# Kernel tuning notes

Hardware: AMD Instinct MI355X
Metric: run time of the kernel (lower is better)

Reference implementation:

```python
import jax, jax.numpy as jnp
import numpy as np

N_HEAD = 16
R = 4  # reciprocal rank

def setup_inputs() -> dict:
    key = jax.random.key(0)
    ks = jax.random.split(key, 8)
    B, T, C = 2, 2048, 1024
    H = N_HEAD
    D = C // H
    D_std = D - R
    x = jax.random.normal(ks[0], (B, T, C), dtype=jnp.float32)
    W_attn = jax.random.normal(ks[1], (3 * C, C), dtype=jnp.float32) * (1.0 / np.sqrt(C))
    W_proj = jax.random.normal(ks[2], (C, C), dtype=jnp.float32) * (1.0 / np.sqrt(C))
    w_std = jnp.full((H,), D_std / D, dtype=jnp.float32)
    w_rec = jnp.full((H,), R / D, dtype=jnp.float32)
    skip_std = jnp.float32(2.0)
    skip_low = jnp.float32(-3.0)
    rwr_alpha = jnp.full((H,), 0.05, dtype=jnp.float32)
    return {"x": x, "W_attn": W_attn, "W_proj": W_proj, "w_std": w_std,
            "w_rec": w_rec, "skip_std": skip_std, "skip_low": skip_low,
            "rwr_alpha": rwr_alpha}

def reference(x, W_attn, W_proj, w_std, w_rec, skip_std, skip_low, rwr_alpha):
    B, T, C = x.shape
    H = N_HEAD
    D = C // H
    D_std = D - R
    # fused QKV projection: [Qf | Kf | V]
    fused = jnp.einsum('btc,fc->btf', x, W_attn)
    qf, kf, v = jnp.split(fused, 3, axis=-1)
    Qf = qf.reshape(B, T, H, D).transpose(0, 2, 1, 3)  # (B,H,T,D)
    Kf = kf.reshape(B, T, H, D).transpose(0, 2, 1, 3)
    V = v.reshape(B, T, H, D).transpose(0, 2, 1, 3)
    # dynamic per-head gate scaling folded into Qf/Kf
    g_std = jnp.sqrt(jnp.clip(w_std * jax.nn.sigmoid(skip_std), 1e-8))  # (H,)
    g_rec = jnp.sqrt(jnp.clip(w_rec * jax.nn.sigmoid(skip_low), 1e-8))  # (H,)
    scale = jnp.concatenate([
        jnp.broadcast_to(g_std[:, None], (H, D_std)),
        jnp.broadcast_to(g_rec[:, None], (H, R)),
    ], axis=-1)  # (H, D)
    scale = scale[None, :, None, :]  # (1,H,1,D)
    Qf = Qf * scale
    Kf = Kf * scale
    # causal SDPA (scale = 1/sqrt(head_dim), dropout=0)
    scores = jnp.einsum('bhqd,bhkd->bhqk', Qf, Kf) / jnp.sqrt(jnp.float32(D))
    causal = jnp.tril(jnp.ones((T, T), dtype=bool))
    scores = jnp.where(causal[None, None], scores, jnp.float32(-1e30))
    attn = jax.nn.softmax(scores, axis=-1)
    y = jnp.einsum('bhqk,bhkd->bhqd', attn, V)
    # self-restart mix: out = (1-alpha)*attn_out + alpha*V, alpha in [0, 0.5]
    alpha = jnp.clip(rwr_alpha, 0.0, 0.5)[None, :, None, None]
    y = (1.0 - alpha) * y + alpha * V
    y = y.transpose(0, 2, 1, 3).reshape(B, T, C)
    return jnp.einsum('btc,oc->bto', y, W_proj)
```

## Files before the change

### kernel.cpp

```cpp
#include <hip/hip_runtime.h>
#include <hip/hip_bf16.h>
#include <math.h>
#include <stdint.h>

#define B_    2
#define T_    2048
#define C_    1024
#define H_    16
#define D_    64
#define R_    4
#define DSTD  60
#define F_    3072
#define BT_   (B_ * T_)

#define LOG2E 1.44269504088896340736f

typedef __bf16 bf16x8 __attribute__((ext_vector_type(8)));
typedef __bf16 bf16x4 __attribute__((ext_vector_type(4)));
typedef float  f32x4  __attribute__((ext_vector_type(4)));

__device__ __forceinline__ int swz(int row, int blk) {
    return blk ^ ((row >> 1) & 7);
}

__device__ __forceinline__ void st_pair(__bf16* p, __bf16 a, __bf16 b) {
    union { __bf16 h[2]; uint32_t u; } t;
    t.h[0] = a; t.h[1] = b;
    *(uint32_t*)p = t.u;
}

__device__ __forceinline__ void gload_lds16(const void* g, void* l) {
    __builtin_amdgcn_global_load_lds(
        (const __attribute__((address_space(1))) uint32_t*)g,
        (__attribute__((address_space(3))) uint32_t*)l, 16, 0, 0);
}

__global__ __launch_bounds__(256) void cast3_kernel(
    const float* __restrict__ a, int na4,
    const float* __restrict__ b, int nb4,
    const float* __restrict__ c, int nc4,
    __bf16* __restrict__ oa, __bf16* __restrict__ ob, __bf16* __restrict__ oc)
{
    int i = blockIdx.x * 256 + threadIdx.x;
    const float* s; __bf16* d; int j = i;
    if (j < na4) { s = a; d = oa; }
    else {
        j -= na4;
        if (j < nb4) { s = b; d = ob; }
        else {
            j -= nb4;
            if (j >= nc4) return;
            s = c; d = oc;
        }
    }
    float4 v = ((const float4*)s)[j];
    bf16x4 o;
    o[0] = (__bf16)v.x; o[1] = (__bf16)v.y;
    o[2] = (__bf16)v.z; o[3] = (__bf16)v.w;
    ((bf16x4*)d)[j] = o;
}

__global__ __launch_bounds__(256) void gemm_qkv_kernel(
    const __bf16* __restrict__ A,
    const __bf16* __restrict__ Bw,
    const float* __restrict__ w_std, const float* __restrict__ w_rec,
    const float* __restrict__ skip_std, const float* __restrict__ skip_low,
    __bf16* __restrict__ Q, __bf16* __restrict__ K, __bf16* __restrict__ V)
{
    __shared__ __bf16 As[128 * 64];
    __shared__ __bf16 Bs[128 * 64];

    const int tid  = threadIdx.x;
    const int row0 = blockIdx.x * 128;
    const int col0 = blockIdx.y * 128;

    const int w    = tid >> 6;
    const int lane = tid & 63;
    const int quad = lane >> 4;
    const int lt   = lane & 15;
    const int wm   = w >> 1;
    const int wn   = w & 1;

    const int srow = tid >> 3;
    const int sblk = tid & 7;

    f32x4 acc[4][4];
#pragma unroll
    for (int i = 0; i < 4; ++i)
#pragma unroll
        for (int j = 0; j < 4; ++j)
#pragma unroll
            for (int r = 0; r < 4; ++r) acc[i][j][r] = 0.f;

    for (int kt = 0; kt < C_ / 64; ++kt) {
        const int k0 = kt * 64;
        __syncthreads();
#pragma unroll
        for (int cc = 0; cc < 4; ++cc) {
            const int r  = cc * 32 + srow;
            const int sb = sblk ^ ((r >> 1) & 7);
            gload_lds16(A  + (size_t)(row0 + r) * C_ + k0 + sb * 8,
                        As + cc * 2048 + tid * 8);
            gload_lds16(Bw + (size_t)(col0 + r) * C_ + k0 + sb * 8,
                        Bs + cc * 2048 + tid * 8);
        }
        __syncthreads();

        bf16x8 waf[2][4], xf[2][4];
#pragma unroll
        for (int kk = 0; kk < 2; ++kk)
#pragma unroll
            for (int i = 0; i < 4; ++i) {
                const int rf = wn * 64 + i * 16 + lt;
                waf[kk][i] = *(const bf16x8*)&Bs[rf * 64 + swz(rf, kk * 4 + quad) * 8];
                const int rt = wm * 64 + i * 16 + lt;
                xf[kk][i]  = *(const bf16x8*)&As[rt * 64 + swz(rt, kk * 4 + quad) * 8];
            }
#pragma unroll
        for (int kk = 0; kk < 2; ++kk)
#pragma unroll
            for (int i = 0; i < 4; ++i)
#pragma unroll
                for (int j = 0; j < 4; ++j)
                    acc[i][j] = __builtin_amdgcn_mfma_f32_16x16x32_bf16(
                        waf[kk][i], xf[kk][j], acc[i][j], 0, 0, 0);
    }

    const int colbase = col0 + wn * 64;
    const int which   = colbase >> 10;
    const int h       = (colbase & (C_ - 1)) >> 6;

    const float ss = 1.f / (1.f + __expf(-skip_std[0]));
    const float sl = 1.f / (1.f + __expf(-skip_low[0]));
    const float gs = sqrtf(fmaxf(w_std[h] * ss, 1e-8f));
    const float gr = sqrtf(fmaxf(w_rec[h] * sl, 1e-8f));

    __bf16* dstM = (which == 0) ? Q : (which == 1) ? K : V;

#pragma unroll
    for (int i = 0; i < 4; ++i) {
        const int d0 = i * 16 + quad * 4;
        float sc = (d0 < DSTD) ? gs : gr;
        if (which == 0) sc *= 0.125f * LOG2E;
        const bool scale = (which != 2);
#pragma unroll
        for (int j = 0; j < 4; ++j) {
            const int trow = row0 + wm * 64 + j * 16 + lt;
            const int b = trow >> 11;
            const int t = trow & (T_ - 1);
            bf16x4 o;
#pragma unroll
            for (int r = 0; r < 4; ++r) {
                float v = acc[i][j][r];
                if (scale) v *= sc;
                o[r] = (__bf16)v;
            }
            *(bf16x4*)(dstM + (((size_t)b * H_ + h) * T_ + t) * D_ + d0) = o;
        }
    }
}

__global__ __launch_bounds__(256) void gemm_out_kernel(
    const __bf16* __restrict__ A,
    const __bf16* __restrict__ Bw,
    float* __restrict__ out)
{
    __shared__ __bf16 As[128 * 64];
    __shared__ __bf16 Bs[64 * 64];

    const int tid  = threadIdx.x;
    const int row0 = blockIdx.x * 128;
    const int col0 = blockIdx.y * 64;

    const int w    = tid >> 6;
    const int lane = tid & 63;
    const int quad = lane >> 4;
    const int lt   = lane & 15;
    const int wm   = w >> 1;
    const int wn   = w & 1;

    const int srow = tid >> 3;
    const int sblk = tid & 7;

    f32x4 acc[2][4];
#pragma unroll
    for (int i = 0; i < 2; ++i)
#pragma unroll
        for (int j = 0; j < 4; ++j)
#pragma unroll
            for (int r = 0; r < 4; ++r) acc[i][j][r] = 0.f;

    for (int kt = 0; kt < C_ / 64; ++kt) {
        const int k0 = kt * 64;
        __syncthreads();
#pragma unroll
        for (int cc = 0; cc < 4; ++cc) {
            const int r  = cc * 32 + srow;
            const int sb = sblk ^ ((r >> 1) & 7);
            gload_lds16(A + (size_t)(row0 + r) * C_ + k0 + sb * 8,
                        As + cc * 2048 + tid * 8);
        }
#pragma unroll
        for (int cc = 0; cc < 2; ++cc) {
            const int r  = cc * 32 + srow;
            const int sb = sblk ^ ((r >> 1) & 7);
            gload_lds16(Bw + (size_t)(col0 + r) * C_ + k0 + sb * 8,
                        Bs + cc * 2048 + tid * 8);
        }
        __syncthreads();

        bf16x8 wpf[2][2], yf[2][4];
#pragma unroll
        for (int kk = 0; kk < 2; ++kk) {
#pragma unroll
            for (int i = 0; i < 2; ++i) {
                const int rb = wn * 32 + i * 16 + lt;
                wpf[kk][i] = *(const bf16x8*)&Bs[rb * 64 + swz(rb, kk * 4 + quad) * 8];
            }
#pragma unroll
            for (int j = 0; j < 4; ++j) {
                const int ra = wm * 64 + j * 16 + lt;
                yf[kk][j] = *(const bf16x8*)&As[ra * 64 + swz(ra, kk * 4 + quad) * 8];
            }
        }
#pragma unroll
        for (int kk = 0; kk < 2; ++kk)
#pragma unroll
            for (int i = 0; i < 2; ++i)
#pragma unroll
                for (int j = 0; j < 4; ++j)
                    acc[i][j] = __builtin_amdgcn_mfma_f32_16x16x32_bf16(
                        wpf[kk][i], yf[kk][j], acc[i][j], 0, 0, 0);
    }

#pragma unroll
    for (int i = 0; i < 2; ++i) {
        const int o = col0 + wn * 32 + i * 16 + quad * 4;
#pragma unroll
        for (int j = 0; j < 4; ++j) {
            const int trow = row0 + wm * 64 + j * 16 + lt;
            float4 v;
            v.x = acc[i][j][0]; v.y = acc[i][j][1];
            v.z = acc[i][j][2]; v.w = acc[i][j][3];
            *(float4*)(out + (size_t)trow * C_ + o) = v;
        }
    }
}

__global__ __launch_bounds__(256) void attn_kernel(
    const __bf16* __restrict__ Q, const __bf16* __restrict__ K,
    const __bf16* __restrict__ V, const float* __restrict__ rwr_alpha,
    __bf16* __restrict__ Y)
{
    __shared__ __align__(16) __bf16 Ks[2][64][64];
    __shared__ __align__(16) __bf16 Vt[2][64][64];
    __shared__ __align__(16) __bf16 Ps[4][16][64];

    const int tid = threadIdx.x;
    const int bh  = blockIdx.x & 31;
    const int g   = blockIdx.x >> 5;
    const int qt  = (g < 8) ? (31 - g) : (g < 16) ? (g - 8)
                  : (g < 24) ? (39 - g) : (g - 16);
    const int h   = bh & (H_ - 1);
    const int b   = bh >> 4;

    const __bf16* Qb = Q + (((size_t)b * H_ + h) * T_) * D_;
    const __bf16* Kb = K + (((size_t)b * H_ + h) * T_) * D_;
    const __bf16* Vb = V + (((size_t)b * H_ + h) * T_) * D_;

    const int w    = tid >> 6;
    const int lane = tid & 63;
    const int quad = lane >> 4;
    const int lt   = lane & 15;

    const int kr0 = tid >> 3;
    const int kc0 = (tid & 7) ^ ((kr0 >> 1) & 7);
    const int kr1 = 32 + kr0;
    const int kc1 = (tid & 7) ^ ((kr1 >> 1) & 7);

    const int kp = (tid >> 3) * 2;
    const int dc = (tid & 7) * 8;
    const int kblk = kp >> 3, koff = kp & 7;

    const __bf16* qrow = Qb + (size_t)(qt * 64 + w * 16 + lt) * D_;
    bf16x8 qf[2];
    qf[0] = *(const bf16x8*)(qrow + quad * 8);
    qf[1] = *(const bf16x8*)(qrow + 32 + quad * 8);

    bf16x8 ones;
#pragma unroll
    for (int u = 0; u < 8; ++u) ones[u] = (__bf16)1.0f;

    gload_lds16(Kb + (size_t)kr0 * 64 + kc0 * 8, &Ks[0][0][0] + tid * 8);
    gload_lds16(Kb + (size_t)kr1 * 64 + kc1 * 8, &Ks[0][32][0] + tid * 8);
    {
        const __bf16* vs = Vb + (size_t)kp * 64 + dc;
        bf16x8 v1 = *(const bf16x8*)(vs);
        bf16x8 v2 = *(const bf16x8*)(vs + 64);
#pragma unroll
        for (int u = 0; u < 8; ++u) {
            const int row = dc + u;
            st_pair(&Vt[0][row][swz(row, kblk) * 8 + koff], v1[u], v2[u]);
        }
    }
    __syncthreads();

    f32x4 lacc;
    f32x4 oacc[4];
#pragma unroll
    for (int r = 0; r < 4; ++r) lacc[r] = 0.f;
#pragma unroll
    for (int n = 0; n < 4; ++n)
#pragma unroll
        for (int r = 0; r < 4; ++r) oacc[n][r] = 0.f;

    for (int kt = 0; kt <= qt; ++kt) {
        const int cur = kt & 1;
        const int nxt = 1 - cur;
        const bool pre = (kt < qt);

        bf16x8 v1, v2;
        if (pre) {
            const size_t toff = (size_t)(kt + 1) * 4096;
            gload_lds16(Kb + toff + (size_t)kr0 * 64 + kc0 * 8, &Ks[nxt][0][0] + tid * 8);
            gload_lds16(Kb + toff + (size_t)kr1 * 64 + kc1 * 8, &Ks[nxt][32][0] + tid * 8);
            const __bf16* vs = Vb + toff + (size_t)kp * 64 + dc;
            v1 = *(const bf16x8*)(vs);
            v2 = *(const bf16x8*)(vs + 64);
        }

        f32x4 sacc[4];
#pragma unroll
        for (int n = 0; n < 4; ++n)
#pragma unroll
            for (int r = 0; r < 4; ++r) sacc[n][r] = 0.f;
        __builtin_amdgcn_s_setprio(1);
#pragma unroll
        for (int kk = 0; kk < 2; ++kk) {
#pragma unroll
            for (int n = 0; n < 4; ++n) {
                const int row = n * 16 + lt;
                bf16x8 ak = *(const bf16x8*)&Ks[cur][row][swz(row, kk * 4 + quad) * 8];
                sacc[n] = __builtin_amdgcn_mfma_f32_16x16x32_bf16(ak, qf[kk], sacc[n], 0, 0, 0);
            }
        }
        __builtin_amdgcn_s_setprio(0);

        if (kt == qt) {
            const int ql = w * 16 + lt;
#pragma unroll
            for (int n = 0; n < 4; ++n) {
                const int keyb = n * 16 + quad * 4;
#pragma unroll
                for (int r = 0; r < 4; ++r)
                    if (keyb + r > ql) sacc[n][r] = -1e30f;
            }
        }

#pragma unroll
        for (int n = 0; n < 4; ++n) {
            bf16x4 pv;
#pragma unroll
            for (int r = 0; r < 4; ++r)
                pv[r] = (__bf16)__builtin_amdgcn_exp2f(sacc[n][r]);
            *(bf16x4*)&Ps[w][lt][swz(lt, n * 2 + (quad >> 1)) * 8 + (quad & 1) * 4] = pv;
        }

        __builtin_amdgcn_s_setprio(1);
#pragma unroll
        for (int kk = 0; kk < 2; ++kk) {
            bf16x8 ap = *(const bf16x8*)&Ps[w][lt][swz(lt, kk * 4 + quad) * 8];
            lacc = __builtin_amdgcn_mfma_f32_16x16x32_bf16(ap, ones, lacc, 0, 0, 0);
#pragma unroll
            for (int nd = 0; nd < 4; ++nd) {
                const int drow = nd * 16 + lt;
                bf16x8 bv = *(const bf16x8*)&Vt[cur][drow][swz(drow, kk * 4 + quad) * 8];
                oacc[nd] = __builtin_amdgcn_mfma_f32_16x16x32_bf16(ap, bv, oacc[nd], 0, 0, 0);
            }
        }
        __builtin_amdgcn_s_setprio(0);

        {
            const float lm = fmaxf(fmaxf(lacc[0], lacc[1]), fmaxf(lacc[2], lacc[3]));
            if (__ballot(lm > 1.0e12f)) {
                const float sc = 1.0f / 4294967296.0f;
#pragma unroll
                for (int r = 0; r < 4; ++r) lacc[r] *= sc;
#pragma unroll
                for (int n = 0; n < 4; ++n)
#pragma unroll
                    for (int r = 0; r < 4; ++r) oacc[n][r] *= sc;
            }
        }

        if (pre) {
#pragma unroll
            for (int u = 0; u < 8; ++u) {
                const int row = dc + u;
                st_pair(&Vt[nxt][row][swz(row, kblk) * 8 + koff], v1[u], v2[u]);
            }
        }
        __syncthreads();
    }

    const float a = fminf(fmaxf(rwr_alpha[h], 0.f), 0.5f);
#pragma unroll
    for (int r = 0; r < 4; ++r) {
        const float inv = 1.f / lacc[r];
        const int qg = qt * 64 + w * 16 + quad * 4 + r;
        const __bf16* vp = Vb + (size_t)qg * D_;
        __bf16* yp = Y + ((size_t)(b * T_ + qg)) * C_ + h * D_;
#pragma unroll
        for (int nd = 0; nd < 4; ++nd) {
            const int d = nd * 16 + lt;
            yp[d] = (__bf16)((1.f - a) * oacc[nd][r] * inv + a * (float)vp[d]);
        }
    }
}

extern "C" void kernel_launch(void* const* d_in, const int* in_sizes, int n_in,
                              void* d_out, int out_size, void* d_ws, size_t ws_size,
                              hipStream_t stream) {
    const float* x        = (const float*)d_in[0];
    const float* W_attn   = (const float*)d_in[1];
    const float* W_proj   = (const float*)d_in[2];
    const float* w_std    = (const float*)d_in[3];
    const float* w_rec    = (const float*)d_in[4];
    const float* skip_std = (const float*)d_in[5];
    const float* skip_low = (const float*)d_in[6];
    const float* rwr      = (const float*)d_in[7];
    float* out = (float*)d_out;

    const size_t nX  = (size_t)BT_ * C_;
    const size_t nWa = (size_t)F_ * C_;
    const size_t nWp = (size_t)C_ * C_;
    const size_t per = (size_t)B_ * H_ * T_ * D_;

    __bf16* xb  = (__bf16*)d_ws;
    __bf16* Wab = xb  + nX;
    __bf16* Wpb = Wab + nWa;
    __bf16* Qb  = Wpb + nWp;
    __bf16* Kb  = Qb  + per;
    __bf16* Vb  = Kb  + per;
    __bf16* Yb  = Vb  + per;

    const int na4 = nX / 4, nb4 = nWa / 4, nc4 = nWp / 4;
    cast3_kernel<<<dim3((na4 + nb4 + nc4 + 255) / 256), 256, 0, stream>>>(
        x, na4, W_attn, nb4, W_proj, nc4, xb, Wab, Wpb);

    gemm_qkv_kernel<<<dim3(BT_ / 128, F_ / 128), 256, 0, stream>>>(
        xb, Wab, w_std, w_rec, skip_std, skip_low, Qb, Kb, Vb);
    attn_kernel<<<dim3(32 * (T_ / 64)), 256, 0, stream>>>(Qb, Kb, Vb, rwr, Yb);
    gemm_out_kernel<<<dim3(BT_ / 128, C_ / 64), 256, 0, stream>>>(Yb, Wpb, out);
}
```

Baseline: 177.9 us.

## Enlarge attention query tile to 128 rows with 512-thread blocks sharing K/V

The attention kernel now handles 128 query rows per block with 8 waves instead of 64 rows with 4 waves. Each staged K/V tile in LDS is reused by twice as many waves, halving global K/V traffic per query. Waves in the lower half skip the final diagonal tile, which adds some idle time and divergence. The grid shrinks to 512 blocks with a new load-balancing order, and the setprio hints are dropped.

```diff
diff --git a/kernel.cpp b/kernel.cpp
--- a/kernel.cpp
+++ b/kernel.cpp
@@ -247,20 +247,19 @@
     }
 }
 
-__global__ __launch_bounds__(256) void attn_kernel(
+__global__ __launch_bounds__(512) void attn_kernel(
     const __bf16* __restrict__ Q, const __bf16* __restrict__ K,
     const __bf16* __restrict__ V, const float* __restrict__ rwr_alpha,
     __bf16* __restrict__ Y)
 {
     __shared__ __align__(16) __bf16 Ks[2][64][64];
     __shared__ __align__(16) __bf16 Vt[2][64][64];
-    __shared__ __align__(16) __bf16 Ps[4][16][64];
+    __shared__ __align__(16) __bf16 Ps[8][16][64];
 
     const int tid = threadIdx.x;
     const int bh  = blockIdx.x & 31;
     const int g   = blockIdx.x >> 5;
-    const int qt  = (g < 8) ? (31 - g) : (g < 16) ? (g - 8)
-                  : (g < 24) ? (39 - g) : (g - 16);
+    const int qb  = (g < 8) ? (15 - g) : (g - 8);
     const int h   = bh & (H_ - 1);
     const int b   = bh >> 4;
 
@@ -273,16 +272,18 @@
     const int quad = lane >> 4;
     const int lt   = lane & 15;
 
-    const int kr0 = tid >> 3;
-    const int kc0 = (tid & 7) ^ ((kr0 >> 1) & 7);
-    const int kr1 = 32 + kr0;
-    const int kc1 = (tid & 7) ^ ((kr1 >> 1) & 7);
-
+    const int kr = tid >> 3;
+    const int kc = (tid & 7) ^ ((kr >> 1) & 7);
+
+    const bool vstg = (tid < 256);
     const int kp = (tid >> 3) * 2;
     const int dc = (tid & 7) * 8;
-    const int kblk = kp >> 3, koff = kp & 7;
-
-    const __bf16* qrow = Qb + (size_t)(qt * 64 + w * 16 + lt) * D_;
+    const int kblk = (kp >> 3) & 7, koff = kp & 7;
+
+    const int ktmax  = 2 * qb + 1;
+    const int tile_w = 2 * qb + (w >> 2);
+
+    const __bf16* qrow = Qb + (size_t)(qb * 128 + w * 16 + lt) * D_;
     bf16x8 qf[2];
     qf[0] = *(const bf16x8*)(qrow + quad * 8);
     qf[1] = *(const bf16x8*)(qrow + 32 + quad * 8);
@@ -291,9 +292,8 @@
 #pragma unroll
     for (int u = 0; u < 8; ++u) ones[u] = (__bf16)1.0f;
 
-    gload_lds16(Kb + (size_t)kr0 * 64 + kc0 * 8, &Ks[0][0][0] + tid * 8);
-    gload_lds16(Kb + (size_t)kr1 * 64 + kc1 * 8, &Ks[0][32][0] + tid * 8);
-    {
+    gload_lds16(Kb + (size_t)kr * 64 + kc * 8, &Ks[0][0][0] + tid * 8);
+    if (vstg) {
         const __bf16* vs = Vb + (size_t)kp * 64 + dc;
         bf16x8 v1 = *(const bf16x8*)(vs);
         bf16x8 v2 = *(const bf16x8*)(vs + 64);
@@ -314,86 +314,86 @@
 #pragma unroll
         for (int r = 0; r < 4; ++r) oacc[n][r] = 0.f;
 
-    for (int kt = 0; kt <= qt; ++kt) {
+    for (int kt = 0; kt <= ktmax; ++kt) {
         const int cur = kt & 1;
         const int nxt = 1 - cur;
-        const bool pre = (kt < qt);
+        const bool pre = (kt < ktmax);
 
         bf16x8 v1, v2;
         if (pre) {
             const size_t toff = (size_t)(kt + 1) * 4096;
-            gload_lds16(Kb + toff + (size_t)kr0 * 64 + kc0 * 8, &Ks[nxt][0][0] + tid * 8);
-            gload_lds16(Kb + toff + (size_t)kr1 * 64 + kc1 * 8, &Ks[nxt][32][0] + tid * 8);
-            const __bf16* vs = Vb + toff + (size_t)kp * 64 + dc;
-            v1 = *(const bf16x8*)(vs);
-            v2 = *(const bf16x8*)(vs + 64);
-        }
-
-        f32x4 sacc[4];
-#pragma unroll
-        for (int n = 0; n < 4; ++n)
-#pragma unroll
-            for (int r = 0; r < 4; ++r) sacc[n][r] = 0.f;
-        __builtin_amdgcn_s_setprio(1);
-#pragma unroll
-        for (int kk = 0; kk < 2; ++kk) {
+            gload_lds16(Kb + toff + (size_t)kr * 64 + kc * 8,
+                        &Ks[nxt][0][0] + tid * 8);
+            if (vstg) {
+                const __bf16* vs = Vb + toff + (size_t)kp * 64 + dc;
+                v1 = *(const bf16x8*)(vs);
+                v2 = *(const bf16x8*)(vs + 64);
+            }
+        }
+
+        if (kt <= tile_w) {
+            f32x4 sacc[4];
+#pragma unroll
+            for (int n = 0; n < 4; ++n)
+#pragma unroll
+                for (int r = 0; r < 4; ++r) sacc[n][r] = 0.f;
+#pragma unroll
+            for (int kk = 0; kk < 2; ++kk) {
+#pragma unroll
+                for (int n = 0; n < 4; ++n) {
+                    const int row = n * 16 + lt;
+                    bf16x8 ak = *(const bf16x8*)&Ks[cur][row][swz(row, kk * 4 + quad) * 8];
+                    sacc[n] = __builtin_amdgcn_mfma_f32_16x16x32_bf16(ak, qf[kk], sacc[n], 0, 0, 0);
+                }
+            }
+
+            if (kt == tile_w) {
+                const int ql = (w & 3) * 16 + lt;
+#pragma unroll
+                for (int n = 0; n < 4; ++n) {
+                    const int keyb = n * 16 + quad * 4;
+#pragma unroll
+                    for (int r = 0; r < 4; ++r)
+                        if (keyb + r > ql) sacc[n][r] = -1e30f;
+                }
+            }
+
 #pragma unroll
             for (int n = 0; n < 4; ++n) {
-                const int row = n * 16 + lt;
-                bf16x8 ak = *(const bf16x8*)&Ks[cur][row][swz(row, kk * 4 + quad) * 8];
-                sacc[n] = __builtin_amdgcn_mfma_f32_16x16x32_bf16(ak, qf[kk], sacc[n], 0, 0, 0);
-            }
-        }
-        __builtin_amdgcn_s_setprio(0);
-
-        if (kt == qt) {
-            const int ql = w * 16 + lt;
-#pragma unroll
-            for (int n = 0; n < 4; ++n) {
-                const int keyb = n * 16 + quad * 4;
+                bf16x4 pv;
 #pragma unroll
                 for (int r = 0; r < 4; ++r)
-                    if (keyb + r > ql) sacc[n][r] = -1e30f;
-            }
-        }
-
-#pragma unroll
-        for (int n = 0; n < 4; ++n) {
-            bf16x4 pv;
-#pragma unroll
-            for (int r = 0; r < 4; ++r)
-                pv[r] = (__bf16)__builtin_amdgcn_exp2f(sacc[n][r]);
-            *(bf16x4*)&Ps[w][lt][swz(lt, n * 2 + (quad >> 1)) * 8 + (quad & 1) * 4] = pv;
-        }
-
-        __builtin_amdgcn_s_setprio(1);
-#pragma unroll
-        for (int kk = 0; kk < 2; ++kk) {
-            bf16x8 ap = *(const bf16x8*)&Ps[w][lt][swz(lt, kk * 4 + quad) * 8];
-            lacc = __builtin_amdgcn_mfma_f32_16x16x32_bf16(ap, ones, lacc, 0, 0, 0);
-#pragma unroll
-            for (int nd = 0; nd < 4; ++nd) {
-                const int drow = nd * 16 + lt;
-                bf16x8 bv = *(const bf16x8*)&Vt[cur][drow][swz(drow, kk * 4 + quad) * 8];
-                oacc[nd] = __builtin_amdgcn_mfma_f32_16x16x32_bf16(ap, bv, oacc[nd], 0, 0, 0);
-            }
-        }
-        __builtin_amdgcn_s_setprio(0);
-
-        {
-            const float lm = fmaxf(fmaxf(lacc[0], lacc[1]), fmaxf(lacc[2], lacc[3]));
-            if (__ballot(lm > 1.0e12f)) {
-                const float sc = 1.0f / 4294967296.0f;
-#pragma unroll
-                for (int r = 0; r < 4; ++r) lacc[r] *= sc;
-#pragma unroll
-                for (int n = 0; n < 4; ++n)
-#pragma unroll
-                    for (int r = 0; r < 4; ++r) oacc[n][r] *= sc;
-            }
-        }
-
-        if (pre) {
+                    pv[r] = (__bf16)__builtin_amdgcn_exp2f(sacc[n][r]);
+                *(bf16x4*)&Ps[w][lt][swz(lt, n * 2 + (quad >> 1)) * 8 + (quad & 1) * 4] = pv;
+            }
+
+#pragma unroll
+            for (int kk = 0; kk < 2; ++kk) {
+                bf16x8 ap = *(const bf16x8*)&Ps[w][lt][swz(lt, kk * 4 + quad) * 8];
+                lacc = __builtin_amdgcn_mfma_f32_16x16x32_bf16(ap, ones, lacc, 0, 0, 0);
+#pragma unroll
+                for (int nd = 0; nd < 4; ++nd) {
+                    const int drow = nd * 16 + lt;
+                    bf16x8 bv = *(const bf16x8*)&Vt[cur][drow][swz(drow, kk * 4 + quad) * 8];
+                    oacc[nd] = __builtin_amdgcn_mfma_f32_16x16x32_bf16(ap, bv, oacc[nd], 0, 0, 0);
+                }
+            }
+
+            {
+                const float lm = fmaxf(fmaxf(lacc[0], lacc[1]), fmaxf(lacc[2], lacc[3]));
+                if (__ballot(lm > 1.0e12f)) {
+                    const float sc = 1.0f / 4294967296.0f;
+#pragma unroll
+                    for (int r = 0; r < 4; ++r) lacc[r] *= sc;
+#pragma unroll
+                    for (int n = 0; n < 4; ++n)
+#pragma unroll
+                        for (int r = 0; r < 4; ++r) oacc[n][r] *= sc;
+                }
+            }
+        }
+
+        if (pre && vstg) {
 #pragma unroll
             for (int u = 0; u < 8; ++u) {
                 const int row = dc + u;
@@ -407,7 +407,7 @@
 #pragma unroll
     for (int r = 0; r < 4; ++r) {
         const float inv = 1.f / lacc[r];
-        const int qg = qt * 64 + w * 16 + quad * 4 + r;
+        const int qg = qb * 128 + w * 16 + quad * 4 + r;
         const __bf16* vp = Vb + (size_t)qg * D_;
         __bf16* yp = Y + ((size_t)(b * T_ + qg)) * C_ + h * D_;
 #pragma unroll
@@ -450,6 +450,6 @@
 
     gemm_qkv_kernel<<<dim3(BT_ / 128, F_ / 128), 256, 0, stream>>>(
         xb, Wab, w_std, w_rec, skip_std, skip_low, Qb, Kb, Vb);
-    attn_kernel<<<dim3(32 * (T_ / 64)), 256, 0, stream>>>(Qb, Kb, Vb, rwr, Yb);
+    attn_kernel<<<dim3(16 * 32), 512, 0, stream>>>(Qb, Kb, Vb, rwr, Yb);
     gemm_out_kernel<<<dim3(BT_ / 128, C_ / 64), 256, 0, stream>>>(Yb, Wpb, out);
 }
```

Measured after the change: 178.0 us. About the same (+0.0%).
